# Kernel optimization log

Measured on AMD Instinct MI355X. Metric: run time of the kernel, lower is better.

The kernel has to match this reference:

```python
import jax, jax.numpy as jnp
from jax import lax
import numpy as np

SIGMA = 25.0
NUM_STEPS = 100
DT = 0.01
SQRT_DT = float(np.sqrt(DT))


def _score(x, eig, t, cond, W1, we, wt, b1, Wc, W2, b2):
    # x: [B,S,H], eig: [B,S], t: scalar, cond: [B,S,H] or None
    h = x @ W1 + eig[..., None] * we + t * wt + b1
    if cond is not None:
        h = h + cond @ Wc
    h = jax.nn.silu(h)
    return h @ W2 + b2


def _diffuse(x_T, eigvals, eigvecs, cond, params, key):
    # reverse SDE from t=1 to t=0 in NUM_STEPS steps
    ts = jnp.linspace(1.0, 0.0, NUM_STEPS)
    keys = jax.random.split(key, NUM_STEPS)
    VT = jnp.swapaxes(eigvecs, -2, -1)  # [B,S,S]

    def step(x, tk):
        t, k = tk
        x_spec = VT @ x                                   # spectral projection [B,S,H]
        score = _score(x_spec, eigvals, t, cond, *params)
        drift = -(SIGMA ** (2.0 * t)) * score
        noise = jax.random.normal(k, x.shape, x.dtype)
        x_new = x - drift * DT + (SIGMA ** t) * SQRT_DT * noise
        return x_new, None

    x, _ = lax.scan(step, x_T, (ts, keys))
    return x


def _make_net(key, H, scale):
    k = jax.random.split(key, 4)
    return dict(
        W1=jax.random.normal(k[0], (H, H), jnp.float32) * scale,
        we=jax.random.normal(k[1], (H,), jnp.float32) * scale,
        wt=jax.random.normal(k[2], (H,), jnp.float32) * scale,
        b1=jnp.zeros((H,), jnp.float32),
        Wc=jax.random.normal(k[3], (H, H), jnp.float32) * scale,
        W2=jax.random.normal(jax.random.fold_in(key, 99), (H, H), jnp.float32) * scale,
        b2=jnp.zeros((H,), jnp.float32),
    )


def setup_inputs() -> dict:
    key = jax.random.key(0)
    B, S, H = 4, 512, 256
    ks = jax.random.split(key, 9)
    inp = {}
    inp['features_text'] = jax.random.normal(ks[0], (B, S, H), jnp.float32)
    inp['features_audio'] = jax.random.normal(ks[1], (B, S, H), jnp.float32)
    inp['features_visual'] = jax.random.normal(ks[2], (B, S, H), jnp.float32)
    sg = jax.random.normal(ks[3], (B, S, S), jnp.float32)
    inp['speaker_graph'] = 0.5 * (sg + jnp.swapaxes(sg, -2, -1))  # symmetric for eigh
    tg = jax.random.normal(ks[4], (B, S, S), jnp.float32)
    inp['temporal_graph'] = 0.5 * (tg + jnp.swapaxes(tg, -2, -1))
    # only text modality (index 0) is missing -> diffusion path for text only
    inp['missing_mask'] = jnp.zeros((B, S, 3), bool).at[:, :, 0].set(True)
    inp['x_T'] = jax.random.normal(ks[5], (B, S, H), jnp.float32)
    scale = 1.0 / np.sqrt(H)
    for prefix, k in [('ts', ks[6]), ('tt', ks[7])]:  # text_speaker / text_temporal nets
        net = _make_net(k, H, scale)
        for name, v in net.items():
            inp[f'{prefix}_{name}'] = v
    kr = jax.random.split(ks[8], 2)
    inp['rec_W'] = jax.random.normal(kr[0], (H, H), jnp.float32) * scale
    inp['rec_b'] = jnp.zeros((H,), jnp.float32)
    return inp


def reference(features_text, features_audio, features_visual,
              speaker_graph, temporal_graph, missing_mask, x_T,
              ts_W1, ts_we, ts_wt, ts_b1, ts_Wc, ts_W2, ts_b2,
              tt_W1, tt_we, tt_wt, tt_b1, tt_Wc, tt_W2, tt_b2,
              rec_W, rec_b):
    # spectral decomposition of both graphs
    s_vals, s_vecs = jnp.linalg.eigh(speaker_graph)
    t_vals, t_vecs = jnp.linalg.eigh(temporal_graph)

    feats = {'text': features_text, 'audio': features_audio, 'visual': features_visual}
    miss = np.asarray(missing_mask)  # concrete branching as in torch forward
    any_missing = [bool(miss[:, :, i].any()) for i in range(3)]

    params = {'text': (
        (ts_W1, ts_we, ts_wt, ts_b1, ts_Wc, ts_W2, ts_b2),
        (tt_W1, tt_we, tt_wt, tt_b1, tt_Wc, tt_W2, tt_b2))}
    key = jax.random.key(42)

    recovered = {}
    for i, modality in enumerate(['text', 'audio', 'visual']):
        if any_missing[i]:
            # condition = mean of present (non-missing) other modalities
            cond_feats = [feats[m] for j, m in enumerate(['text', 'audio', 'visual'])
                          if m != modality and not any_missing[j]]
            cond = None
            if cond_feats:
                cond = jnp.mean(jnp.stack(cond_feats, axis=-1), axis=-1)
            k_s, k_t = jax.random.split(jax.random.fold_in(key, i))
            p_s, p_t = params[modality]
            x_s = _diffuse(x_T, s_vals, s_vecs, cond, p_s, k_s)
            x_t = _diffuse(x_T, t_vals, t_vecs, cond, p_t, k_t)
            rec = 0.5 * (x_s + x_t)
            recovered[modality] = rec @ rec_W + rec_b
        else:
            recovered[modality] = feats[modality]
    return (recovered['text'], recovered['audio'], recovered['visual'])
```

## Files before the change

kernel.cpp:

```cpp
#include <hip/hip_runtime.h>
#include <math.h>
#include <stdint.h>


#define NT 256
#define SZF 131072
#define MATSZ 262144
#define NB 16
#define ILAST 384
#define TBASE (ILAST+1)
#define TSZ (512-TBASE)

#define BD_DK   0
#define BD_ZK   4096
#define BD_RZK  8192
#define BD_TAU  12288
#define BD_DS   16384
#define BD_RHO  20480
#define BD_KSK  20736
#define BD_KIDX 22784
#define BD_DIDX 24832
#define BD_PERM 26880
#define BD_CNT  28928

#define ALD(p)    __hip_atomic_load((p),  __ATOMIC_RELAXED, __HIP_MEMORY_SCOPE_AGENT)
#define AST(p,v)  __hip_atomic_store((p), (v), __ATOMIC_RELAXED, __HIP_MEMORY_SCOPE_AGENT)

__host__ __device__ static inline unsigned rotl32(unsigned v, int r){ return (v<<r)|(v>>(32-r)); }

__host__ __device__ static inline void tf2x32(unsigned k0, unsigned k1,
                                              unsigned x0, unsigned x1,
                                              unsigned* o0, unsigned* o1){
  unsigned ks2 = k0 ^ k1 ^ 0x1BD11BDAu;
  x0 += k0; x1 += k1;
#define TF4(r0,r1,r2,r3) \
  x0 += x1; x1 = rotl32(x1,r0); x1 ^= x0; \
  x0 += x1; x1 = rotl32(x1,r1); x1 ^= x0; \
  x0 += x1; x1 = rotl32(x1,r2); x1 ^= x0; \
  x0 += x1; x1 = rotl32(x1,r3); x1 ^= x0;
  TF4(13,15,26,6)  x0 += k1;  x1 += ks2 + 1u;
  TF4(17,29,16,24) x0 += ks2; x1 += k0 + 2u;
  TF4(13,15,26,6)  x0 += k0;  x1 += k1 + 3u;
  TF4(17,29,16,24) x0 += k1;  x1 += ks2 + 4u;
  TF4(13,15,26,6)  x0 += ks2; x1 += k0 + 5u;
#undef TF4
  *o0 = x0; *o1 = x1;
}

__device__ static inline float erfinv_xla(float x){
  float w = -log1pf(-x*x);
  float p;
  if (w < 5.0f){
    w -= 2.5f;
    p = 2.81022636e-08f;
    p = fmaf(p, w, 3.43273939e-07f);
    p = fmaf(p, w, -3.5233877e-06f);
    p = fmaf(p, w, -4.39150654e-06f);
    p = fmaf(p, w, 0.00021858087f);
    p = fmaf(p, w, -0.00125372503f);
    p = fmaf(p, w, -0.00417768164f);
    p = fmaf(p, w, 0.246640727f);
    p = fmaf(p, w, 1.50140941f);
  } else {
    w = sqrtf(w) - 3.0f;
    p = -0.000200214257f;
    p = fmaf(p, w, 0.000100950558f);
    p = fmaf(p, w, 0.00134934322f);
    p = fmaf(p, w, -0.00367342844f);
    p = fmaf(p, w, 0.00573950773f);
    p = fmaf(p, w, -0.0076224613f);
    p = fmaf(p, w, 0.00943887047f);
    p = fmaf(p, w, 1.00167406f);
    p = fmaf(p, w, 2.83297682f);
  }
  return p*x;
}

__device__ static inline float bits_to_normal(unsigned bits){
  const float MINV = -0.99999994f;
  float f = __uint_as_float((bits >> 9) | 0x3f800000u) - 1.0f;
  float u = fmaxf(MINV, fmaf(f, 2.0f, MINV));
  return 1.41421356237309515f * erfinv_xla(u);
}

__device__ __forceinline__ void gbar2(unsigned* slots, int sg, int g, unsigned epoch,
                                      int* sdead){
  __threadfence_block();
  __syncthreads();
  int t = threadIdx.x;
  if (t == 0) AST(slots + (sg*NB + g)*16, epoch);
  if (t < NB && !*sdead){
    unsigned* sl = slots + (sg*NB + t)*16;
    int spins = 0;
    while (ALD(sl) < epoch){
      if (++spins > (1<<24)){ *sdead = 1; break; }
      if ((spins & 3) == 0) __builtin_amdgcn_s_sleep(1);
    }
  }
  __syncthreads();
}

__global__ __launch_bounds__(256) void k_sytd2_lds(const float* Gs, const float* Gt,
                                                   double* Vb, double* smalls,
                                                   unsigned* slots, double* Atail){
  int sg = blockIdx.x / NB, g = blockIdx.x % NB;
  const float* G = (sg < 4) ? (Gs + (size_t)sg*MATSZ) : (Gt + (size_t)(sg-4)*MATSZ);
  double* V = Vb + (size_t)sg*MATSZ;
  double* d  = smalls + (size_t)sg*512;
  double* e  = smalls + 4096 + (size_t)sg*512;
  double* tu = smalls + 8192 + (size_t)sg*512;
  double* acc0 = smalls + 274688 + (size_t)sg*512;
  double* acc1 = acc0 + 4096;
  double* col0 = smalls + 282880 + (size_t)sg*512;
  double* col1 = col0 + 4096;
  double* vvh  = smalls + 291072 + (size_t)sg*512;
  double* At = Atail + (size_t)sg*MATSZ;
  int t = threadIdx.x, wave = t >> 6, lane = t & 63;

  __shared__ double Arows[32][512];
  __shared__ double vv[512], wv[512], col2[512], acc[512];
  __shared__ double red[4];
  __shared__ double bc[4];
  __shared__ int sdead;

  if (t == 0) sdead = 0;

  for (int j=0; j<32; j++){
    int r = NB*j + g;
    for (int c=t; c<512; c+=256)
      Arows[j][c] = (double)G[(size_t)r*512 + c];
  }

  for (int r=t; r<512; r+=256) col2[r] = (r>=1) ? (double)G[(size_t)r*512] : 0.0;
  __syncthreads();
  {
    double part = 0.0;
    for (int r=2+t; r<512; r+=256) part += col2[r]*col2[r];
    #pragma unroll
    for (int off=32; off; off>>=1) part += __shfl_down(part, off, 64);
    if (lane==0) red[wave]=part;
    __syncthreads();
    if (t==0){
      double xsq = red[0]+red[1]+red[2]+red[3];
      double alpha = col2[1];
      double beta,tv,scal;
      if (xsq == 0.0){ beta=alpha; tv=0.0; scal=0.0; }
      else {
        beta = -copysign(sqrt(alpha*alpha + xsq), alpha);
        tv = (beta - alpha)/beta;
        scal = 1.0/(alpha - beta);
      }
      if (g==0){ e[0]=beta; tu[0]=tv; }
      bc[0]=tv; bc[1]=scal;
    }
  }
  __syncthreads();
  double tauv = bc[0];
  {
    double scal = bc[1];
    for (int r=t; r<512; r+=256){
      double v = 0.0;
      if (r==1) v = 1.0;
      else if (r>1) v = (tauv==0.0) ? 0.0 : col2[r]*scal;
      vv[r]=v;
      if (r>=1 && (r & (NB-1))==g) V[r] = v;
    }
  }
  __syncthreads();
  if (g==0){
    for (int r=1+t; r<512; r+=256) AST(&col0[r], (double)G[(size_t)r*512 + 1]);
  }
  {
    int r0 = 1 + ((g - 1) & (NB-1));
    for (int r = r0 + NB*wave; r < 512; r += 4*NB){
      const double* Ar = Arows[r>>4];
      double p = 0.0;
      for (int c=lane; c<512; c+=64) p += Ar[c]*vv[c];
      #pragma unroll
      for (int off=32; off; off>>=1) p += __shfl_down(p, off, 64);
      if (lane==0) AST(&acc0[r], p);
    }
  }

  for (int i=0; i<ILAST; i++){
    gbar2(slots, sg, g, (unsigned)(i+1), &sdead);
    int lo=i+1, lo2=i+2;
    double* accR = (i&1) ? acc1 : acc0;
    double* colR = (i&1) ? col1 : col0;
    double* accW = (i&1) ? acc0 : acc1;
    double* colW = (i&1) ? col0 : col1;
    double part = 0.0;
    for (int r=lo+t; r<512; r+=256){
      double a_ = ALD(&accR[r]);
      double c_ = ALD(&colR[r]);
      acc[r]=a_; col2[r]=c_;
      part += (tauv*a_)*vv[r];
    }
    #pragma unroll
    for (int off=32; off; off>>=1) part += __shfl_down(part, off, 64);
    if (lane==0) red[wave]=part;
    __syncthreads();
    {
      double dot = red[0]+red[1]+red[2]+red[3];
      double alpha2 = -0.5*tauv*dot;
      double vlo = vv[lo];
      double wlo = fma(alpha2, vlo, tauv*acc[lo]);
      for (int r=lo+t; r<512; r+=256){
        double wr = fma(alpha2, vv[r], tauv*acc[r]);
        wv[r]=wr;
        col2[r] = col2[r] - vv[r]*wlo - wr*vlo;
      }
    }
    __syncthreads();
    part = 0.0;
    for (int r=lo2+1+t; r<512; r+=256) part += col2[r]*col2[r];
    #pragma unroll
    for (int off=32; off; off>>=1) part += __shfl_down(part, off, 64);
    if (lane==0) red[wave]=part;
    __syncthreads();
    double tau2, scal2;
    {
      double xsq = red[0]+red[1]+red[2]+red[3];
      double alpha = col2[lo2];
      double beta;
      if (xsq == 0.0){ beta=alpha; tau2=0.0; scal2=0.0; }
      else {
        beta = -copysign(sqrt(alpha*alpha + xsq), alpha);
        tau2 = (beta - alpha)/beta;
        scal2 = 1.0/(alpha - beta);
      }
      if (t==0 && g==0){ e[lo]=beta; tu[lo]=tau2; }
    }
    {
      double vvc[8], wvc[8], v2c[8];
      #pragma unroll
      for (int j=0;j<8;j++){
        int c = lo + lane + 64*j;
        bool ok = c < 512;
        vvc[j] = ok ? vv[c] : 0.0;
        wvc[j] = ok ? wv[c] : 0.0;
        double v2v = 0.0;
        if (ok){
          if (c==lo2) v2v = 1.0;
          else if (c>lo2) v2v = (tau2==0.0) ? 0.0 : col2[c]*scal2;
        }
        v2c[j] = v2v;
      }
      int r0 = lo + ((g - lo) & (NB-1));
      for (int r = r0 + NB*wave; r < 512; r += 4*NB){
        double* Ar = Arows[r>>4];
        double vr = vv[r], wr = wv[r];
        double p = 0.0;
        #pragma unroll
        for (int j=0;j<8;j++){
          int c = lo + lane + 64*j;
          if (c < 512){
            double an = Ar[c] - vr*wvc[j] - wr*vvc[j];
            Ar[c] = an;
            p += an * v2c[j];
            if (c == lo2) AST(&colW[r], an);
          }
        }
        #pragma unroll
        for (int off=32; off; off>>=1) p += __shfl_down(p, off, 64);
        if (lane==0) AST(&accW[r], p);
      }
    }
    __syncthreads();
    for (int r=t; r<512; r+=256){
      double v = 0.0;
      if (r==lo2) v = 1.0;
      else if (r>lo2) v = (tau2==0.0) ? 0.0 : col2[r]*scal2;
      vv[r]=v;
      if (r>=lo2 && (r & (NB-1))==g) V[(size_t)lo*512 + r] = v;
    }
    tauv = tau2;
  }

  if (t < 32){
    int r = NB*t + g;
    if (r <= ILAST) d[r] = Arows[t][r];
  }
  for (int j=0; j<32; j++){
    int r = NB*j + g;
    if (r >= TBASE){
      for (int c=TBASE+t; c<512; c+=256)
        At[(size_t)r*512 + c] = Arows[j][c];
    }
  }
  if (g==0){
    for (int r=t; r<512; r+=256) vvh[r] = vv[r];
  }
}

__global__ __launch_bounds__(256) void k_sy_tail(const double* Atail, double* Vb,
                                                 double* smalls){
  int sg = blockIdx.x;
  double* V = Vb + (size_t)sg*MATSZ;
  double* d  = smalls + (size_t)sg*512;
  double* e  = smalls + 4096 + (size_t)sg*512;
  double* tu = smalls + 8192 + (size_t)sg*512;
  const double* accG = smalls + 274688 + (size_t)sg*512;
  const double* colG = smalls + 282880 + (size_t)sg*512;
  const double* vvG  = smalls + 291072 + (size_t)sg*512;
  const double* At0 = Atail + (size_t)sg*MATSZ;
  int t = threadIdx.x, wave = t >> 6, lane = t & 63;

  __shared__ double At[TSZ*128];
  __shared__ double vv[512], wv[512], col2[512], acc[512], accN[512], colN[512];
  __shared__ double red[4];

  for (int rl=0; rl<TSZ; rl++)
    for (int cl=t; cl<TSZ; cl+=256)
      At[rl*128+cl] = At0[(size_t)(TBASE+rl)*512 + TBASE+cl];
  for (int r=t; r<512; r+=256){
    if (r >= ILAST){ vv[r]=vvG[r]; acc[r]=accG[r]; col2[r]=colG[r]; }
  }
  double tauv = tu[ILAST];
  __syncthreads();

  for (int i=ILAST; i<510; i++){
    int lo=i+1, lo2=i+2;
    double part = 0.0;
    for (int r=lo+t; r<512; r+=256) part += (tauv*acc[r])*vv[r];
    #pragma unroll
    for (int off=32; off; off>>=1) part += __shfl_down(part, off, 64);
    if (lane==0) red[wave]=part;
    __syncthreads();
    {
      double dot = red[0]+red[1]+red[2]+red[3];
      double alpha2 = -0.5*tauv*dot;
      double vlo = vv[lo];
      double wlo = fma(alpha2, vlo, tauv*acc[lo]);
      for (int r=lo+t; r<512; r+=256){
        double wr = fma(alpha2, vv[r], tauv*acc[r]);
        wv[r]=wr;
        col2[r] = col2[r] - vv[r]*wlo - wr*vlo;
      }
    }
    __syncthreads();
    part = 0.0;
    for (int r=lo2+1+t; r<512; r+=256) part += col2[r]*col2[r];
    #pragma unroll
    for (int off=32; off; off>>=1) part += __shfl_down(part, off, 64);
    if (lane==0) red[wave]=part;
    __syncthreads();
    double tau2, scal2;
    {
      double xsq = red[0]+red[1]+red[2]+red[3];
      double alpha = col2[lo2];
      double beta;
      if (xsq == 0.0){ beta=alpha; tau2=0.0; scal2=0.0; }
      else {
        beta = -copysign(sqrt(alpha*alpha + xsq), alpha);
        tau2 = (beta - alpha)/beta;
        scal2 = 1.0/(alpha - beta);
      }
      if (t==0){ e[lo]=beta; tu[lo]=tau2; }
    }
    {
      double vvc[8], wvc[8], v2c[8];
      #pragma unroll
      for (int j=0;j<8;j++){
        int c = lo + lane + 64*j;
        bool ok = c < 512;
        vvc[j] = ok ? vv[c] : 0.0;
        wvc[j] = ok ? wv[c] : 0.0;
        double v2v = 0.0;
        if (ok){
          if (c==lo2) v2v = 1.0;
          else if (c>lo2) v2v = (tau2==0.0) ? 0.0 : col2[c]*scal2;
        }
        v2c[j] = v2v;
      }
      for (int r = lo + wave; r < 512; r += 4){
        double* Ar = &At[(r-TBASE)*128];
        double vr = vv[r], wr = wv[r];
        double p = 0.0;
        #pragma unroll
        for (int j=0;j<8;j++){
          int c = lo + lane + 64*j;
          if (c < 512){
            double an = Ar[c-TBASE] - vr*wvc[j] - wr*vvc[j];
            Ar[c-TBASE] = an;
            p += an * v2c[j];
            if (c == lo2) colN[r] = an;
          }
        }
        #pragma unroll
        for (int off=32; off; off>>=1) p += __shfl_down(p, off, 64);
        if (lane==0) accN[r] = p;
      }
    }
    __syncthreads();
    for (int r=t; r<512; r+=256){
      if (r >= lo2){
        double v = (r==lo2) ? 1.0 : ((tau2==0.0) ? 0.0 : col2[r]*scal2);
        vv[r]=v;
        V[(size_t)lo*512 + r] = v;
        col2[r] = colN[r];
        acc[r] = accN[r];
      }
    }
    tauv = tau2;
    __syncthreads();
  }
  for (int rl=t; rl<TSZ; rl+=256) d[TBASE+rl] = At[rl*128+rl];
}

__global__ void k_scale(double* smalls, int sbase){
  int sg = sbase + blockIdx.x, t = threadIdx.x;
  double* d = smalls + (size_t)sg*512;
  double* e = smalls + 4096 + (size_t)sg*512;
  __shared__ double red[256];
  double m = 0.0;
  for (int i=t;i<512;i+=256) m = fmax(m, fabs(d[i]));
  for (int i=t;i<511;i+=256) m = fmax(m, fabs(e[i]));
  red[t]=m; __syncthreads();
  for (int off=128; off; off>>=1){ if (t<off) red[t]=fmax(red[t],red[t+off]); __syncthreads(); }
  double org = red[0]; if (org == 0.0) org = 1.0;
  if (t==0) smalls[12288+sg] = org;
  double inv = 1.0/org;
  __syncthreads();
  for (int i=t;i<512;i+=256) d[i] *= inv;
  for (int i=t;i<511;i+=256) e[i] *= inv;
  __syncthreads();
  if (t < 31){
    int k = t + 1;
    double ae = fabs(e[16*k - 1]);
    d[16*k - 1] -= ae;
    d[16*k]     -= ae;
  }
}

__global__ __launch_bounds__(256) void k_leaves(double* smalls, double* Zb, int sbase){
  __shared__ double LA[4][256];
  __shared__ double LQ[4][256];
  int t = threadIdx.x, w = t >> 6, lane = t & 63;
  int L = blockIdx.x*4 + w;
  int s_local = L >> 5;
  int sg = sbase + s_local;
  int leaf = L & 31;
  double* dd = smalls + (size_t)sg*512;
  double* ee = smalls + 4096 + (size_t)sg*512;
  double* Z = Zb + (size_t)s_local*MATSZ;
  int base = leaf*16;
  double* A = LA[w]; double* Q = LQ[w];

  for (int i=lane; i<256; i+=64){ A[i]=0.0; Q[i]=0.0; }
  __builtin_amdgcn_sched_barrier(0);
  if (lane < 16){ A[lane*17] = dd[base+lane]; Q[lane*17] = 1.0; }
  if (lane < 15){
    double ev = ee[base+lane];
    A[lane*16+lane+1] = ev; A[(lane+1)*16+lane] = ev;
  }
  __builtin_amdgcn_sched_barrier(0);
  double nr = 0.0;
  if (lane == 0){ for (int i=0;i<256;i++) nr += A[i]*A[i]; }
  nr = __shfl(nr, 0, 64);
  double thr = nr*1e-30 + 1e-300;

  for (int sweep=0; sweep<60; sweep++){
    double offs = 0.0;
    for (int p=0;p<15;p++) for (int q=p+1;q<16;q++){
      double apq = A[p*16+q];
      offs += 2.0*apq*apq;
      if (apq == 0.0) continue;
      double theta = 0.5*(A[q*17]-A[p*17])/apq;
      double tt;
      if (fabs(theta) > 1e18) tt = 0.5/theta;
      else tt = copysign(1.0, theta)/(fabs(theta)+sqrt(theta*theta+1.0));
      double cc = 1.0/sqrt(tt*tt+1.0), ss = tt*cc;
      __builtin_amdgcn_sched_barrier(0);
      if (lane < 16){
        int k = lane;
        double akp=A[k*16+p], akq=A[k*16+q];
        A[k*16+p] = cc*akp - ss*akq;
        A[k*16+q] = ss*akp + cc*akq;
      }
      __builtin_amdgcn_sched_barrier(0);
      if (lane < 16){
        int k = lane;
        double apk=A[p*16+k], aqk=A[q*16+k];
        A[p*16+k] = cc*apk - ss*aqk;
        A[q*16+k] = ss*apk + cc*aqk;
      }
      __builtin_amdgcn_sched_barrier(0);
      if (lane < 16){
        int k = lane;
        double qkp=Q[k*16+p], qkq=Q[k*16+q];
        Q[k*16+p] = cc*qkp - ss*qkq;
        Q[k*16+q] = ss*qkp + cc*qkq;
      }
      __builtin_amdgcn_sched_barrier(0);
    }
    if (offs < thr) break;
  }
  __builtin_amdgcn_sched_barrier(0);
  if (lane == 0){
    for (int i=0;i<16;i++){
      int mi=i;
      for (int j=i+1;j<16;j++) if (A[j*17] < A[mi*17]) mi=j;
      if (mi!=i){
        double tmp=A[i*17]; A[i*17]=A[mi*17]; A[mi*17]=tmp;
        for (int k=0;k<16;k++){ double q1=Q[k*16+i]; Q[k*16+i]=Q[k*16+mi]; Q[k*16+mi]=q1; }
      }
    }
  }
  __builtin_amdgcn_sched_barrier(0);
  if (lane < 16) dd[base+lane] = A[lane*17];
  for (int i=lane; i<256; i+=64){
    int r = i >> 4, c = i & 15;
    Z[(size_t)(base+r)*512 + base + c] = Q[i];
  }
}

__global__ __launch_bounds__(256) void k_deflate(double* smalls, const double* Zsrc_b,
                                                 double* bscr, int level, int sbase){
  const double EPS32 = 5.9604644775390625e-8;
  const double ISQ2  = 0.70710678118654752440;
  int s_local = blockIdx.x;
  int sg = sbase + s_local;
  int hh = 16 << level, n = hh << 1;
  int merge = blockIdx.y, start = merge*n;
  double* d = smalls + (size_t)sg*512;
  const double* e = smalls + 4096 + (size_t)sg*512;
  const double* Z = Zsrc_b + (size_t)s_local*MATSZ;
  double* rotg = smalls + 12544 + (size_t)(sg*32+merge)*1024;
  double* dkG  = bscr + BD_DK  + (size_t)s_local*512 + start;
  double* zkG  = bscr + BD_ZK  + (size_t)s_local*512 + start;
  double* rzkG = bscr + BD_RZK + (size_t)s_local*512 + start;
  double* dsG  = bscr + BD_DS  + (size_t)s_local*512 + start;
  double* rhoG = bscr + BD_RHO;
  int* kidxG = (int*)(bscr + BD_KIDX) + s_local*512 + start;
  int* didxG = (int*)(bscr + BD_DIDX) + s_local*512 + start;
  int* permG = (int*)(bscr + BD_PERM) + s_local*512 + start;
  int* cntG  = (int*)(bscr + BD_CNT) + (s_local*32+merge)*2;

  __shared__ double ds[512], zl[512];
  __shared__ double rc[256], rs[256];
  __shared__ double red[256];
  __shared__ double sv[2];
  __shared__ int perm[512], kidx[512], didx[512];
  __shared__ int rp[256], rq[256];
  __shared__ int counts[2];
  int t = threadIdx.x;
  if (t == 0){
    int i=0, j=hh, k=0;
    while (i < hh && j < n){
      if (d[start+i] <= d[start+j]) perm[k++]=i++; else perm[k++]=j++;
    }
    while (i < hh) perm[k++]=i++;
    while (j < n)  perm[k++]=j++;
  }
  __syncthreads();
  double eb = e[start+hh-1];
  double rho = 2.0*fabs(eb);
  double sgn = (eb < 0.0) ? -1.0 : 1.0;
  for (int i=t; i<n; i+=NT){
    int p = perm[i];
    ds[i] = d[start+p];
    double zr = (p < hh) ? Z[(size_t)(start+hh-1)*512 + start + p]
                         : sgn * Z[(size_t)(start+hh)*512 + start + p];
    zl[i] = zr * ISQ2;
  }
  __syncthreads();
  double m = 0.0;
  for (int i=t;i<n;i+=NT) m = fmax(m, fabs(zl[i]));
  red[t]=m; __syncthreads();
  for (int off=128; off; off>>=1){ if (t<off) red[t]=fmax(red[t],red[t+off]); __syncthreads(); }
  if (t==0) sv[0] = red[0];
  __syncthreads();
  m = 0.0;
  for (int i=t;i<n;i+=NT) m = fmax(m, fabs(ds[i]));
  red[t]=m; __syncthreads();
  for (int off=128; off; off>>=1){ if (t<off) red[t]=fmax(red[t],red[t+off]); __syncthreads(); }
  if (t==0) sv[1] = red[0];
  __syncthreads();
  double zmaxv = sv[0];
  double tol = 8.0*EPS32*fmax(sv[1], zmaxv);

  if (t == 0){
    int K=0, nd=0, nrot=0;
    if (rho*zmaxv <= tol){
      for (int j=0;j<n;j++) didx[nd++]=j;
    } else {
      int pj = -1;
      for (int j=0;j<n;j++){
        if (rho*fabs(zl[j]) <= tol){
          didx[nd++]=j;
        } else if (pj < 0){
          pj = j;
        } else {
          double s_ = zl[pj], c_ = zl[j];
          double tau2 = sqrt(c_*c_ + s_*s_);
          double tdf = ds[j] - ds[pj];
          double cc = c_/tau2, sr = -s_/tau2;
          if (fabs(tdf*cc*sr) <= tol){
            zl[j] = tau2; zl[pj] = 0.0;
            if (nrot < 256){
              rp[nrot]=perm[pj]; rq[nrot]=perm[j]; rc[nrot]=cc; rs[nrot]=sr; nrot++;
            }
            double tn = ds[pj]*cc*cc + ds[j]*sr*sr;
            ds[j]  = ds[pj]*sr*sr + ds[j]*cc*cc;
            ds[pj] = tn;
            didx[nd++] = pj;
            pj = j;
          } else {
            kidx[K++] = pj;
            pj = j;
          }
        }
      }
      if (pj >= 0) kidx[K++] = pj;
    }
    for (int a=1;a<nd;a++){
      int v = didx[a]; double dv = ds[v]; int b = a-1;
      while (b >= 0 && ds[didx[b]] > dv){ didx[b+1]=didx[b]; b--; }
      didx[b+1] = v;
    }
    counts[0]=K; counts[1]=nd;
    cntG[0]=K; cntG[1]=nd;
    rhoG[s_local*32+merge] = rho;
    rotg[0] = (double)nrot;
    for (int i=0;i<nrot;i++){
      rotg[1+4*i]=(double)rp[i]; rotg[2+4*i]=(double)rq[i];
      rotg[3+4*i]=rc[i]; rotg[4+4*i]=rs[i];
    }
  }
  __syncthreads();
  int K = counts[0], nd = counts[1];
  for (int k=t; k<K; k+=NT){
    int ki = kidx[k];
    double dv = ds[ki], zv = zl[ki];
    dkG[k]=dv; zkG[k]=zv; rzkG[k]=(rho*zv)*zv; kidxG[k]=ki;
  }
  for (int j=t; j<n;  j+=NT){ dsG[j]=ds[j]; permG[j]=perm[j]; }
  for (int j=t; j<nd; j+=NT) didxG[j]=didx[j];
}

__global__ __launch_bounds__(256) void k_bisect(double* bscr, int level, int split){
  int s_local = blockIdx.x;
  int hh = 16 << level, n = hh << 1;
  int merge = blockIdx.y, start = merge*n;
  const double* dkG  = bscr + BD_DK  + (size_t)s_local*512 + start;
  const double* zkG  = bscr + BD_ZK  + (size_t)s_local*512 + start;
  const double* rzkG = bscr + BD_RZK + (size_t)s_local*512 + start;
  double* taukG = bscr + BD_TAU + (size_t)s_local*512 + start;
  int* KskG = (int*)(bscr + BD_KSK) + s_local*512 + start;
  const int* cntG = (int*)(bscr + BD_CNT) + (s_local*32+merge)*2;
  double rho = (bscr + BD_RHO)[s_local*32+merge];
  __shared__ double dks[512], rzks[512], zks[512];
  int t = threadIdx.x;
  int K = cntG[0];
  for (int i=t;i<K;i+=NT){ dks[i]=dkG[i]; rzks[i]=rzkG[i]; zks[i]=zkG[i]; }
  __syncthreads();
  int lane = t & 63, w = t >> 6;
  for (int j2 = blockIdx.z*4 + w; j2 < K; j2 += split*4){
    int Kb; double lo, hi;
    if (j2 < K-1){
      double mid = 0.5*(dks[j2+1]-dks[j2]);
      double dj = dks[j2];
      double part = 0.0;
      for (int i=lane;i<K;i+=64){ double dif=(dks[i]-dj)-mid; part += rzks[i]/dif; }
      #pragma unroll
      for (int off=32; off; off>>=1) part += __shfl_xor(part, off, 64);
      double gg = 1.0 + part;
      if (gg >= 0.0){ Kb=j2;   lo=0.0;  hi=mid; }
      else          { Kb=j2+1; lo=-mid; hi=0.0; }
    } else {
      double part = 0.0;
      for (int i=lane;i<K;i+=64) part += zks[i]*zks[i];
      #pragma unroll
      for (int off=32; off; off>>=1) part += __shfl_xor(part, off, 64);
      Kb=K-1; lo=0.0; hi=rho*part + 1e-300;
    }
    double dK = dks[Kb];
    for (int it=0; it<72; it++){
      double mid = 0.5*(lo+hi);
      if (mid==lo || mid==hi) break;
      double part = 0.0;
      for (int i=lane;i<K;i+=64){ double dif=(dks[i]-dK)-mid; part += rzks[i]/dif; }
      #pragma unroll
      for (int off=32; off; off>>=1) part += __shfl_xor(part, off, 64);
      double gg = 1.0 + part;
      if (gg < 0.0) lo=mid; else hi=mid;
    }
    if (lane==0){ KskG[j2]=Kb; taukG[j2]=0.5*(lo+hi); }
  }
}

__global__ __launch_bounds__(256) void k_sfin(double* smalls, double* Sm_b,
                                              const double* bscr, int level, int sbase){
  int s_local = blockIdx.x;
  int sg = sbase + s_local;
  int hh = 16 << level, n = hh << 1;
  int merge = blockIdx.y, start = merge*n;
  double* d = smalls + (size_t)sg*512;
  double* Sm = Sm_b + (size_t)s_local*MATSZ;
  const double* rotg = smalls + 12544 + (size_t)(sg*32+merge)*1024;
  const double* dkG  = bscr + BD_DK  + (size_t)s_local*512 + start;
  const double* zkG  = bscr + BD_ZK  + (size_t)s_local*512 + start;
  const double* taukG= bscr + BD_TAU + (size_t)s_local*512 + start;
  const double* dsG  = bscr + BD_DS  + (size_t)s_local*512 + start;
  const int* KskG = (int*)(bscr + BD_KSK) + s_local*512 + start;
  const int* kidxG= (int*)(bscr + BD_KIDX) + s_local*512 + start;
  const int* didxG= (int*)(bscr + BD_DIDX) + s_local*512 + start;
  const int* permG= (int*)(bscr + BD_PERM) + s_local*512 + start;
  const int* cntG = (int*)(bscr + BD_CNT) + (s_local*32+merge)*2;
  double rho = (bscr + BD_RHO)[s_local*32+merge];
  __shared__ double dk[512], zk[512], tauk[512], zh[512], outlam[512], ds[512];
  __shared__ int Ksk[512], kidx[512], didx[512], perm[512], outid[512];
  int t = threadIdx.x;
  int K = cntG[0], nd = cntG[1];
  for (int i=t;i<K;i+=NT){
    dk[i]=dkG[i]; zk[i]=zkG[i]; tauk[i]=taukG[i]; Ksk[i]=KskG[i]; kidx[i]=kidxG[i];
  }
  for (int i=t;i<n;i+=NT){ ds[i]=dsG[i]; perm[i]=permG[i]; }
  for (int i=t;i<nd;i+=NT) didx[i]=didxG[i];
  __syncthreads();
  for (int i=t; i<K; i+=NT){
    double P = (Ksk[i]==i) ? tauk[i] : (dk[Ksk[i]]-dk[i]) + tauk[i];
    for (int j=0;j<K;j++){
      if (j==i) continue;
      double num = (dk[Ksk[j]]-dk[i]) + tauk[j];
      double den = dk[j]-dk[i];
      P *= num/den;
    }
    zh[i] = copysign(sqrt(fabs(P/rho)), zk[i]);
  }
  __syncthreads();
  if (t == 0){
    int a=0, b=0;
    for (int j=0;j<n;j++){
      double la = (a<K)  ? (dk[Ksk[a]]+tauk[a]) : 1e300;
      double lb = (b<nd) ? ds[didx[b]]          : 1e300;
      if (la <= lb){ outid[j]=a;     outlam[j]=la; a++; }
      else         { outid[j]=512+b; outlam[j]=lb; b++; }
    }
  }
  __syncthreads();
  for (int j=t; j<n; j+=NT) d[start+j] = outlam[j];
  for (int j=t; j<n; j+=NT){
    double* col = Sm + (size_t)(start+j)*512;
    int id = outid[j];
    for (int i=0;i<n;i++) col[i]=0.0;
    if (id >= 512){
      col[perm[didx[id-512]]] = 1.0;
    } else {
      int k = id;
      double ss_ = 0.0;
      for (int i=0;i<K;i++){
        double dif = (dk[i]-dk[Ksk[k]]) - tauk[k];
        if (dif == 0.0) dif = 1e-300;
        double v = zh[i]/dif;
        col[perm[kidx[i]]] = v; ss_ += v*v;
      }
      double inv = 1.0/sqrt(ss_);
      for (int i=0;i<K;i++) col[perm[kidx[i]]] *= inv;
    }
  }
  int cnt = (int)rotg[0];
  if (cnt > 0){
    for (int j=t; j<n; j+=NT){
      double* col = Sm + (size_t)(start+j)*512;
      for (int i=cnt-1; i>=0; i--){
        int p = (int)rotg[1+4*i], q = (int)rotg[2+4*i];
        double c = rotg[3+4*i], sr = rotg[4+4*i];
        double a = col[p], b = col[q];
        col[p] = c*a - sr*b;
        col[q] = sr*a + c*b;
      }
    }
  }
}

__global__ __launch_bounds__(256) void k_gemm64(const double* Zsrc_b, const double* Sm_b,
                                                double* Zdst_b, int level){
  int hh = 16 << level, n = hh << 1;
  int mpm = 512 / n;
  int bz = blockIdx.z;
  int s = bz / mpm, merge = bz % mpm;
  int start = merge*n;
  const double* Zs = Zsrc_b + (size_t)s*MATSZ;
  const double* Sm = Sm_b + (size_t)s*MATSZ;
  double* Zd = Zdst_b + (size_t)s*MATSZ;
  int row0 = start + blockIdx.y*32, col0 = start + blockIdx.x*32;
  int t = threadIdx.x;
  int tr = t >> 4, tc = t & 15;
  __shared__ double As[32][33];
  __shared__ double Bs[32][33];
  double a00=0,a01=0,a10=0,a11=0;
  for (int q0=0; q0<n; q0+=32){
    #pragma unroll
    for (int it=0; it<4; it++){
      int idx = t + it*256;
      int r = idx >> 5, q = idx & 31;
      As[r][q] = Zs[(size_t)(row0+r)*512 + start + q0 + q];
    }
    #pragma unroll
    for (int it=0; it<4; it++){
      int idx = t + it*256;
      int c = idx >> 5, q = idx & 31;
      Bs[q][c] = Sm[(size_t)(col0+c)*512 + q0 + q];
    }
    __syncthreads();
    #pragma unroll 8
    for (int q=0;q<32;q++){
      double ar0=As[tr][q], ar1=As[tr+16][q];
      double bc0=Bs[q][tc], bc1=Bs[q][tc+16];
      a00 = fma(ar0,bc0,a00); a01 = fma(ar0,bc1,a01);
      a10 = fma(ar1,bc0,a10); a11 = fma(ar1,bc1,a11);
    }
    __syncthreads();
  }
  Zd[(size_t)(row0+tr)*512 + col0+tc]       = a00;
  Zd[(size_t)(row0+tr)*512 + col0+tc+16]    = a01;
  Zd[(size_t)(row0+tr+16)*512 + col0+tc]    = a10;
  Zd[(size_t)(row0+tr+16)*512 + col0+tc+16] = a11;
}

__global__ __launch_bounds__(256) void k_backq(double* Z2_b, const double* Vh_b,
                                               const double* smalls, int sbase){
  int s_local = blockIdx.x, cb = blockIdx.y;
  int sg = sbase + s_local;
  double* Z = Z2_b + (size_t)s_local*MATSZ;
  const double* V = Vh_b + (size_t)sg*MATSZ;
  const double* tu = smalls + 8192 + (size_t)sg*512;
  int cg = threadIdx.x >> 5, lane = threadIdx.x & 31;
  int c = cb*8 + cg;
  __shared__ double zc[8][512];
  for (int r=lane; r<512; r+=32) zc[cg][r] = Z[(size_t)r*512 + c];
  for (int i=509; i>=0; i--){
    double tv = tu[i];
    if (tv == 0.0) continue;
    double wp = 0.0;
    for (int r=i+1+lane; r<512; r+=32) wp += V[(size_t)i*512 + r]*zc[cg][r];
    #pragma unroll
    for (int off=16; off; off>>=1) wp += __shfl_down(wp, off, 32);
    double w = __shfl(wp, 0, 32);
    double tw = tv*w;
    for (int r=i+1+lane; r<512; r+=32) zc[cg][r] -= tw*V[(size_t)i*512 + r];
  }
  for (int r=lane; r<512; r+=32) Z[(size_t)r*512 + c] = zc[cg][r];
}

__global__ void k_finalize(const double* Z2_b, const double* smalls,
                           float* Vs32, float* Vt32, float* eig, int sbase){
  int s_local = blockIdx.x;
  int sg = sbase + s_local;
  const double* Z = Z2_b + (size_t)s_local*MATSZ;
  float* Vt_pass = (sg < 4) ? (Vs32 + (size_t)sg*MATSZ)
                            : (Vt32 + (size_t)(sg-4)*MATSZ);
  double org = smalls[12288+sg];
  int idx = blockIdx.y*256 + threadIdx.x;
  int r = idx >> 9, c = idx & 511;
  Vt_pass[(size_t)c*512 + r] = (float)Z[(size_t)r*512 + c];
  if (idx < 512)
    eig[(size_t)sg*512 + idx] = (float)(smalls[(size_t)sg*512 + idx]*org);
}

struct KArgs {
  const float* Vt;
  const float* Vt2;
  float *xspec, *hbuf, *x, *E;
  const float *W1s, *W1t, *W2s, *W2t;
  const float *b2s, *b2t, *wts, *wtt, *b1s, *b1t, *wes, *wet;
  const float *cond, *Wcs, *Wct;
  const float *eig;
  const float *rec, *recW, *recb;
  float* out;
  float t, a, bc;
  unsigned nk0, nk1, nk2, nk3;
  int mode, nmat, ntx;
};

__global__ __launch_bounds__(256) void k_gemm32(KArgs P){
  int t = threadIdx.x;
  int L = blockIdx.x;
  int mat = L % P.nmat;
  int tile = L / P.nmat;
  int n0 = (tile % P.ntx) << 5;
  int m0 = (tile / P.ntx) << 6;
  const float *A, *B; float *C;
  int lda, K, chain = 0;
  if (P.mode == 0){
    A = (mat < 4) ? (P.Vt + (size_t)mat*MATSZ) : (P.Vt2 + (size_t)(mat-4)*MATSZ);
    lda = 512; K = 512;
    B = P.x + (size_t)mat*SZF; C = P.xspec + (size_t)mat*SZF;
  } else if (P.mode == 1){
    chain = mat >> 2;
    A = P.xspec + (size_t)mat*SZF; lda = 256; K = 256;
    B = chain ? P.W1t : P.W1s; C = P.hbuf + (size_t)mat*SZF;
  } else if (P.mode == 2){
    chain = mat >> 2;
    A = P.hbuf + (size_t)mat*SZF; lda = 256; K = 256;
    B = chain ? P.W2t : P.W2s; C = P.x + (size_t)mat*SZF;
  } else if (P.mode == 3){
    chain = mat;
    A = P.cond; lda = 256; K = 256;
    B = chain ? P.Wct : P.Wcs; C = P.E + (size_t)chain*4*SZF;
  } else {
    A = P.rec; lda = 256; K = 256;
    B = P.recW; C = P.out;
  }
  __shared__ float As[2][32][68];
  __shared__ float Bs[2][32][36];
  float acc[4][2] = {{0}};
  const int ra = t >> 2, kk4 = (t & 3) << 2;
  const int kb = (t & 127) >> 3, c4 = (t & 7) << 2;
  const int tr4 = (t >> 4) << 2, tc2 = (t & 15) << 1;
  const float* Aptr = &A[(size_t)(m0 + ra)*lda + kk4];
  const float* Bptr = &B[(size_t)kb*256 + n0 + c4];
  {
    const float4 av  = *(const float4*)Aptr;
    const float4 av2 = *(const float4*)(Aptr + 16);
    As[0][kk4+0][ra]=av.x;  As[0][kk4+1][ra]=av.y;  As[0][kk4+2][ra]=av.z;  As[0][kk4+3][ra]=av.w;
    As[0][16+kk4+0][ra]=av2.x; As[0][16+kk4+1][ra]=av2.y; As[0][16+kk4+2][ra]=av2.z; As[0][16+kk4+3][ra]=av2.w;
    if (t < 128){
      const float4 bv  = *(const float4*)Bptr;
      const float4 bv2 = *(const float4*)(Bptr + (size_t)16*256);
      *(float4*)&Bs[0][kb][c4] = bv;
      *(float4*)&Bs[0][kb+16][c4] = bv2;
    }
  }
  int buf = 0;
  for (int k0=0; k0<K; k0+=32){
    __syncthreads();
    bool more = (k0+32) < K;
    float4 avN, avN2, bvN, bvN2;
    if (more){
      avN  = *(const float4*)(Aptr + k0 + 32);
      avN2 = *(const float4*)(Aptr + k0 + 48);
      if (t < 128){
        bvN  = *(const float4*)(Bptr + (size_t)(k0+32)*256);
        bvN2 = *(const float4*)(Bptr + (size_t)(k0+48)*256);
      }
    }
    {
      const float (*Asb)[68] = As[buf];
      const float (*Bsb)[36] = Bs[buf];
      #pragma unroll
      for (int kk=0; kk<32; kk++){
        const float4 a4 = *(const float4*)&Asb[kk][tr4];
        const float2 b2 = *(const float2*)&Bsb[kk][tc2];
        const float ar[4] = {a4.x, a4.y, a4.z, a4.w};
        #pragma unroll
        for (int q=0;q<4;q++){
          acc[q][0] = fmaf(ar[q], b2.x, acc[q][0]);
          acc[q][1] = fmaf(ar[q], b2.y, acc[q][1]);
        }
      }
    }
    if (more){
      int nb = buf^1;
      As[nb][kk4+0][ra]=avN.x;  As[nb][kk4+1][ra]=avN.y;  As[nb][kk4+2][ra]=avN.z;  As[nb][kk4+3][ra]=avN.w;
      As[nb][16+kk4+0][ra]=avN2.x; As[nb][16+kk4+1][ra]=avN2.y; As[nb][16+kk4+2][ra]=avN2.z; As[nb][16+kk4+3][ra]=avN2.w;
      if (t < 128){
        *(float4*)&Bs[nb][kb][c4] = bvN;
        *(float4*)&Bs[nb][kb+16][c4] = bvN2;
      }
      buf = nb;
    }
  }
  #pragma unroll
  for (int q=0;q<4;q++){
    int r = m0 + tr4 + q;
    size_t rowoff = (size_t)r*256 + n0 + tc2;
    float2 cv;
    if (P.mode == 2) cv = *(const float2*)&C[rowoff];
    float res[2];
    #pragma unroll
    for (int p=0;p<2;p++){
      int c = n0 + tc2 + p;
      size_t oi = (size_t)r*256 + c;
      float v = acc[q][p];
      if (P.mode == 1){
        v += P.E[(size_t)mat*SZF + oi] + P.t * ((chain ? P.wtt : P.wts)[c]);
        float sg = 1.0f/(1.0f + expf(-v));
        v = v * sg;
      } else if (P.mode == 2){
        float bias = (chain ? P.b2t : P.b2s)[c];
        unsigned j = ((unsigned)(mat & 3))*131072u + (unsigned)oi;
        unsigned kk0 = chain ? P.nk2 : P.nk0;
        unsigned kk1 = chain ? P.nk3 : P.nk1;
        unsigned y0, y1;
        tf2x32(kk0, kk1, 0u, j, &y0, &y1);
        float nz = bits_to_normal(y0 ^ y1);
        float cx = (p==0) ? cv.x : cv.y;
        v = cx + P.a*(v + bias) + P.bc*nz;
      } else if (P.mode == 3){
        int bb = r >> 9, s2 = r & 511;
        v += (chain ? P.b1t : P.b1s)[c]
           + P.eig[(size_t)(chain*4 + bb)*512 + s2] * ((chain ? P.wet : P.wes)[c]);
      } else if (P.mode == 4){
        v += P.recb[c];
      }
      res[p] = v;
    }
    *(float2*)&C[rowoff] = make_float2(res[0], res[1]);
  }
}

__global__ void k_init(float* cond, float* x, const float* a, const float* v,
                       const float* xT){
  size_t i = (size_t)blockIdx.x*256 + threadIdx.x;
  size_t b = i >> 17, off = i & 131071;
  x[i] = xT[((b & 3) << 17) + off];
  if (i < 524288) cond[i] = 0.5f*(a[i] + v[i]);
}

__global__ void k_recc(float* rec, const float* x, float* out,
                       const float* a, const float* v){
  size_t i = (size_t)blockIdx.x*256 + threadIdx.x;
  if (i < 524288) rec[i] = 0.5f*(x[i] + x[i + 524288]);
  out[524288 + i] = (i < 524288) ? a[i] : v[i - 524288];
}

extern "C" void kernel_launch(void* const* d_in, const int* in_sizes, int n_in,
                              void* d_out, int out_size, void* d_ws, size_t ws_size,
                              hipStream_t stream){
  const float* f_audio   = (const float*)d_in[1];
  const float* f_visual  = (const float*)d_in[2];
  const float* g_speaker = (const float*)d_in[3];
  const float* g_temporal= (const float*)d_in[4];
  const float* x_T       = (const float*)d_in[6];
  const float* tsW1=(const float*)d_in[7],  *tswe=(const float*)d_in[8],
             * tswt=(const float*)d_in[9],  *tsb1=(const float*)d_in[10],
             * tsWc=(const float*)d_in[11], *tsW2=(const float*)d_in[12],
             * tsb2=(const float*)d_in[13];
  const float* ttW1=(const float*)d_in[14], *ttwe=(const float*)d_in[15],
             * ttwt=(const float*)d_in[16], *ttb1=(const float*)d_in[17],
             * ttWc=(const float*)d_in[18], *ttW2=(const float*)d_in[19],
             * ttb2=(const float*)d_in[20];
  const float* recW=(const float*)d_in[21], *recb=(const float*)d_in[22];
  float* out = (float*)d_out;

  const size_t MB = 1ull << 20;
  if (ws_size < 43*MB) return;
  bool wide = ws_size >= 80*MB;

  char* ws = (char*)d_ws;
  double* Vh     = (double*)(ws + 0);
  double* Atail  = (double*)(ws + 16*MB);
  double* A64    = (double*)(ws + 16*MB);
  double* Zb     = wide ? (double*)(ws + 48*MB) : (double*)(ws + 24*MB);
  double* Sm     = wide ? (double*)(ws + 64*MB) : (double*)(ws + 32*MB);
  double* smalls = (double*)(ws + 40*MB);
  unsigned* slots = (unsigned*)(smalls + 295168);
  float* Vt32_s  = (float*)(ws + 0);
  float* Vt32_t  = (float*)(ws + 8*MB);
  float* eig32   = (float*)(ws + 42*MB + 512*1024);
  double* bscr   = (double*)(ws + 42*MB + 640*1024);
  float* cond  = (float*)(ws + 16*MB);
  float* E     = (float*)(ws + 18*MB);
  float* xall  = (float*)(ws + 22*MB);
  float* xspec = (float*)(ws + 26*MB);
  float* hbuf  = (float*)(ws + 30*MB);

  unsigned f0, f1;
  tf2x32(0u, 42u, 0u, 0u, &f0, &f1);
  unsigned s0,s1,t0,t1;
  tf2x32(f0, f1, 0u, 0u, &s0, &s1);
  tf2x32(f0, f1, 0u, 1u, &t0, &t1);
  unsigned skeys[100][2], tkeys[100][2];
  for (int k=0; k<100; k++){
    tf2x32(s0, s1, 0u, (unsigned)k, &skeys[k][0], &skeys[k][1]);
    tf2x32(t0, t1, 0u, (unsigned)k, &tkeys[k][0], &tkeys[k][1]);
  }

  hipMemsetAsync(slots, 0, 16384, stream);

  k_sytd2_lds<<<8*NB, 256, 0, stream>>>(g_speaker, g_temporal, Vh, smalls, slots, Atail);
  k_sy_tail<<<8, 256, 0, stream>>>(Atail, Vh, smalls);

  int npass = wide ? 1 : 2;
  int nmat  = wide ? 8 : 4;
  for (int pass=0; pass<npass; pass++){
    int sbase = wide ? 0 : 4*pass;
    k_scale<<<nmat, 256, 0, stream>>>(smalls, sbase);
    hipMemsetAsync(Zb, 0, (size_t)(wide?16:8)*MB, stream);
    hipMemsetAsync(A64, 0, (size_t)(wide?16:8)*MB, stream);
    k_leaves<<<nmat*8, 256, 0, stream>>>(smalls, Zb, sbase);
    for (int level=0; level<5; level++){
      int n = 32 << level, mpm = 512/n;
      double* src = (level & 1) ? A64 : Zb;
      double* dst = (level & 1) ? Zb  : A64;
      int split = 2 << level;
      k_deflate<<<dim3(nmat, mpm), 256, 0, stream>>>(smalls, src, bscr, level, sbase);
      k_bisect<<<dim3(nmat, mpm, split), 256, 0, stream>>>(bscr, level, split);
      k_sfin<<<dim3(nmat, mpm), 256, 0, stream>>>(smalls, Sm, bscr, level, sbase);
      k_gemm64<<<dim3(n/32, n/32, nmat*mpm), 256, 0, stream>>>(src, Sm, dst, level);
    }
    k_backq<<<dim3(nmat, 64), 256, 0, stream>>>(A64, Vh, smalls, sbase);
    k_finalize<<<dim3(nmat, 1024), 256, 0, stream>>>(A64, smalls,
                                                     Vt32_s, Vt32_t, eig32, sbase);
  }

  k_init<<<4096, 256, 0, stream>>>(cond, xall, f_audio, f_visual, x_T);

  KArgs P;
  P.Vt = Vt32_s; P.Vt2 = Vt32_t;
  P.xspec = xspec; P.hbuf = hbuf; P.x = xall; P.E = E;
  P.W1s = tsW1; P.W1t = ttW1; P.W2s = tsW2; P.W2t = ttW2;
  P.b2s = tsb2; P.b2t = ttb2; P.wts = tswt; P.wtt = ttwt;
  P.b1s = tsb1; P.b1t = ttb1; P.wes = tswe; P.wet = ttwe;
  P.cond = cond; P.Wcs = tsWc; P.Wct = ttWc;
  P.eig = eig32; P.rec = xspec; P.recW = recW; P.recb = recb; P.out = out;
  P.t = 0.f; P.a = 0.f; P.bc = 0.f;
  P.nk0 = 0; P.nk1 = 0; P.nk2 = 0; P.nk3 = 0;
  P.ntx = 8;

  P.mode = 3; P.nmat = 2;
  k_gemm32<<<512, 256, 0, stream>>>(P);

  for (int k=0; k<100; k++){
    float tf = (float)(1.0 - (double)k/99.0);
    float av = (float)(pow(25.0, 2.0*(double)tf) * 0.01);
    float bcv = (float)(pow(25.0, (double)tf) * 0.1);
    P.nk0 = skeys[k][0]; P.nk1 = skeys[k][1];
    P.nk2 = tkeys[k][0]; P.nk3 = tkeys[k][1];
    P.nmat = 8;
    P.mode = 0;
    k_gemm32<<<512, 256, 0, stream>>>(P);
    P.mode = 1; P.t = tf;
    k_gemm32<<<512, 256, 0, stream>>>(P);
    P.mode = 2; P.a = av; P.bc = bcv;
    k_gemm32<<<512, 256, 0, stream>>>(P);
  }

  k_recc<<<4096, 256, 0, stream>>>(xspec, xall, out, f_audio, f_visual);
  P.mode = 4; P.nmat = 1;
  k_gemm32<<<256, 256, 0, stream>>>(P);
}
```

Before: 14.17 ms.

## Fuse score MLP GEMMs into one kernel and tile the eigvec transpose

Replaces the two per-step GEMM launches (x_spec@W1 with SiLU, then h@W2 with noise update) with one fused kernel. Each block keeps an 8-row strip of x_spec and the hidden activations in LDS, so the hidden buffer never goes to global memory. It also rewrites the finalize transpose to use a 32x32 LDS tile for coalesced writes, and merges the Givens rotation loop into the eigenvector-construction loop. The tradeoff is lower parallelism per block: 8 rows per block, with W1/W2 re-streamed by every block.

Result: slower. 18.03 ms (+27.2%).

```diff
diff --git a/kernel.cpp b/kernel.cpp
--- a/kernel.cpp
+++ b/kernel.cpp
@@ -741,6 +741,7 @@
   }
   __syncthreads();
   for (int j=t; j<n; j+=NT) d[start+j] = outlam[j];
+  int cnt = (int)rotg[0];
   for (int j=t; j<n; j+=NT){
     double* col = Sm + (size_t)(start+j)*512;
     int id = outid[j];
@@ -759,18 +760,12 @@
       double inv = 1.0/sqrt(ss_);
       for (int i=0;i<K;i++) col[perm[kidx[i]]] *= inv;
     }
-  }
-  int cnt = (int)rotg[0];
-  if (cnt > 0){
-    for (int j=t; j<n; j+=NT){
-      double* col = Sm + (size_t)(start+j)*512;
-      for (int i=cnt-1; i>=0; i--){
-        int p = (int)rotg[1+4*i], q = (int)rotg[2+4*i];
-        double c = rotg[3+4*i], sr = rotg[4+4*i];
-        double a = col[p], b = col[q];
-        col[p] = c*a - sr*b;
-        col[q] = sr*a + c*b;
-      }
+    for (int i=cnt-1; i>=0; i--){
+      int p = (int)rotg[1+4*i], q = (int)rotg[2+4*i];
+      double c = rotg[3+4*i], sr = rotg[4+4*i];
+      double a = col[p], b = col[q];
+      col[p] = c*a - sr*b;
+      col[q] = sr*a + c*b;
     }
   }
 }
@@ -852,26 +847,42 @@
   const double* Z = Z2_b + (size_t)s_local*MATSZ;
   float* Vt_pass = (sg < 4) ? (Vs32 + (size_t)sg*MATSZ)
                             : (Vt32 + (size_t)(sg-4)*MATSZ);
-  double org = smalls[12288+sg];
-  int idx = blockIdx.y*256 + threadIdx.x;
-  int r = idx >> 9, c = idx & 511;
-  Vt_pass[(size_t)c*512 + r] = (float)Z[(size_t)r*512 + c];
-  if (idx < 512)
-    eig[(size_t)sg*512 + idx] = (float)(smalls[(size_t)sg*512 + idx]*org);
+  int t = threadIdx.x;
+  int tr = blockIdx.y & 15, tc = blockIdx.y >> 4;
+  __shared__ float ft[32][33];
+  {
+    int i = t >> 3, j4 = (t & 7) << 2;
+    const double* zr = &Z[(size_t)(tr*32 + i)*512 + tc*32 + j4];
+    ft[i][j4+0] = (float)zr[0];
+    ft[i][j4+1] = (float)zr[1];
+    ft[i][j4+2] = (float)zr[2];
+    ft[i][j4+3] = (float)zr[3];
+  }
+  __syncthreads();
+  {
+    int j = t >> 3, i4 = (t & 7) << 2;
+    float* vr = &Vt_pass[(size_t)(tc*32 + j)*512 + tr*32 + i4];
+    vr[0] = ft[i4+0][j];
+    vr[1] = ft[i4+1][j];
+    vr[2] = ft[i4+2][j];
+    vr[3] = ft[i4+3][j];
+  }
+  if (blockIdx.y == 0){
+    double org = smalls[12288+sg];
+    for (int idx=t; idx<512; idx+=256)
+      eig[(size_t)sg*512 + idx] = (float)(smalls[(size_t)sg*512 + idx]*org);
+  }
 }
 
 struct KArgs {
   const float* Vt;
   const float* Vt2;
-  float *xspec, *hbuf, *x, *E;
-  const float *W1s, *W1t, *W2s, *W2t;
-  const float *b2s, *b2t, *wts, *wtt, *b1s, *b1t, *wes, *wet;
+  float *xspec, *x, *E;
+  const float *b1s, *b1t, *wes, *wet;
   const float *cond, *Wcs, *Wct;
   const float *eig;
   const float *rec, *recW, *recb;
   float* out;
-  float t, a, bc;
-  unsigned nk0, nk1, nk2, nk3;
   int mode, nmat, ntx;
 };
 
@@ -888,14 +899,6 @@
     A = (mat < 4) ? (P.Vt + (size_t)mat*MATSZ) : (P.Vt2 + (size_t)(mat-4)*MATSZ);
     lda = 512; K = 512;
     B = P.x + (size_t)mat*SZF; C = P.xspec + (size_t)mat*SZF;
-  } else if (P.mode == 1){
-    chain = mat >> 2;
-    A = P.xspec + (size_t)mat*SZF; lda = 256; K = 256;
-    B = chain ? P.W1t : P.W1s; C = P.hbuf + (size_t)mat*SZF;
-  } else if (P.mode == 2){
-    chain = mat >> 2;
-    A = P.hbuf + (size_t)mat*SZF; lda = 256; K = 256;
-    B = chain ? P.W2t : P.W2s; C = P.x + (size_t)mat*SZF;
   } else if (P.mode == 3){
     chain = mat;
     A = P.cond; lda = 256; K = 256;
@@ -967,29 +970,12 @@
   for (int q=0;q<4;q++){
     int r = m0 + tr4 + q;
     size_t rowoff = (size_t)r*256 + n0 + tc2;
-    float2 cv;
-    if (P.mode == 2) cv = *(const float2*)&C[rowoff];
     float res[2];
     #pragma unroll
     for (int p=0;p<2;p++){
       int c = n0 + tc2 + p;
-      size_t oi = (size_t)r*256 + c;
       float v = acc[q][p];
-      if (P.mode == 1){
-        v += P.E[(size_t)mat*SZF + oi] + P.t * ((chain ? P.wtt : P.wts)[c]);
-        float sg = 1.0f/(1.0f + expf(-v));
-        v = v * sg;
-      } else if (P.mode == 2){
-        float bias = (chain ? P.b2t : P.b2s)[c];
-        unsigned j = ((unsigned)(mat & 3))*131072u + (unsigned)oi;
-        unsigned kk0 = chain ? P.nk2 : P.nk0;
-        unsigned kk1 = chain ? P.nk3 : P.nk1;
-        unsigned y0, y1;
-        tf2x32(kk0, kk1, 0u, j, &y0, &y1);
-        float nz = bits_to_normal(y0 ^ y1);
-        float cx = (p==0) ? cv.x : cv.y;
-        v = cx + P.a*(v + bias) + P.bc*nz;
-      } else if (P.mode == 3){
+      if (P.mode == 3){
         int bb = r >> 9, s2 = r & 511;
         v += (chain ? P.b1t : P.b1s)[c]
            + P.eig[(size_t)(chain*4 + bb)*512 + s2] * ((chain ? P.wet : P.wes)[c]);
@@ -999,6 +985,148 @@
       res[p] = v;
     }
     *(float2*)&C[rowoff] = make_float2(res[0], res[1]);
+  }
+}
+
+struct KFuse {
+  const float *xspec, *E;
+  float* x;
+  const float *W1s, *W1t, *W2s, *W2t;
+  const float *b2s, *b2t, *wts, *wtt;
+  float t, a, bc;
+  unsigned nk0, nk1, nk2, nk3;
+};
+
+__global__ __launch_bounds__(256) void k_fuse12(KFuse S){
+  int t = threadIdx.x;
+  int mat = blockIdx.x & 7;
+  int row0 = (blockIdx.x >> 3) << 3;
+  int chain = mat >> 2;
+  const float* xsp_g = S.xspec + (size_t)mat*SZF;
+  float* xg = S.x + (size_t)mat*SZF;
+  const float* W1 = chain ? S.W1t : S.W1s;
+  const float* W2 = chain ? S.W2t : S.W2s;
+  const float* Eb = S.E + (size_t)mat*SZF;
+  const float* wt = chain ? S.wtt : S.wts;
+  const float* b2 = chain ? S.b2t : S.b2s;
+
+  __shared__ float xs[8][264];
+  __shared__ float hl[8][264];
+  __shared__ float Bt[2][16][264];
+
+  const int kb = t >> 4, cb = (t & 15) << 4;
+  const int rr = t >> 5, c4 = (t & 31) << 2;
+
+  {
+    float4 v0 = *(const float4*)&xsp_g[(size_t)(row0 + rr)*256 + c4];
+    float4 v1 = *(const float4*)&xsp_g[(size_t)(row0 + rr)*256 + c4 + 128];
+    *(float4*)&xs[rr][c4] = v0;
+    *(float4*)&xs[rr][c4+128] = v1;
+  }
+  #pragma unroll
+  for (int j=0;j<4;j++)
+    *(float4*)&Bt[0][kb][cb + 4*j] = *(const float4*)&W1[(size_t)kb*256 + cb + 4*j];
+
+  float acc[8];
+  #pragma unroll
+  for (int j=0;j<8;j++) acc[j]=0.f;
+  int cur = 0;
+  for (int k0=0; k0<256; k0+=16){
+    __syncthreads();
+    bool more = (k0+16) < 256;
+    float4 pw[4];
+    if (more){
+      #pragma unroll
+      for (int j=0;j<4;j++)
+        pw[j] = *(const float4*)&W1[(size_t)(k0+16+kb)*256 + cb + 4*j];
+    }
+    #pragma unroll
+    for (int kk=0; kk<16; kk++){
+      float a = xs[rr][k0+kk];
+      const float4 b0 = *(const float4*)&Bt[cur][kk][c4];
+      const float4 b1 = *(const float4*)&Bt[cur][kk][c4+128];
+      acc[0]=fmaf(a,b0.x,acc[0]); acc[1]=fmaf(a,b0.y,acc[1]);
+      acc[2]=fmaf(a,b0.z,acc[2]); acc[3]=fmaf(a,b0.w,acc[3]);
+      acc[4]=fmaf(a,b1.x,acc[4]); acc[5]=fmaf(a,b1.y,acc[5]);
+      acc[6]=fmaf(a,b1.z,acc[6]); acc[7]=fmaf(a,b1.w,acc[7]);
+    }
+    if (more){
+      int nb = cur^1;
+      #pragma unroll
+      for (int j=0;j<4;j++) *(float4*)&Bt[nb][kb][cb+4*j] = pw[j];
+      cur = nb;
+    }
+  }
+  {
+    int rg = row0 + rr;
+    const float4 e0 = *(const float4*)&Eb[(size_t)rg*256 + c4];
+    const float4 e1 = *(const float4*)&Eb[(size_t)rg*256 + c4 + 128];
+    const float ev[8] = {e0.x,e0.y,e0.z,e0.w,e1.x,e1.y,e1.z,e1.w};
+    #pragma unroll
+    for (int j=0;j<8;j++){
+      int c = (j<4) ? (c4 + j) : (c4 + 128 + j - 4);
+      float v = acc[j];
+      v += ev[j] + S.t * wt[c];
+      float sg = 1.0f/(1.0f + expf(-v));
+      hl[rr][c] = v * sg;
+    }
+  }
+  __syncthreads();
+  #pragma unroll
+  for (int j=0;j<4;j++)
+    *(float4*)&Bt[0][kb][cb + 4*j] = *(const float4*)&W2[(size_t)kb*256 + cb + 4*j];
+  #pragma unroll
+  for (int j=0;j<8;j++) acc[j]=0.f;
+  cur = 0;
+  for (int k0=0; k0<256; k0+=16){
+    __syncthreads();
+    bool more = (k0+16) < 256;
+    float4 pw[4];
+    if (more){
+      #pragma unroll
+      for (int j=0;j<4;j++)
+        pw[j] = *(const float4*)&W2[(size_t)(k0+16+kb)*256 + cb + 4*j];
+    }
+    #pragma unroll
+    for (int kk=0; kk<16; kk++){
+      float a = hl[rr][k0+kk];
+      const float4 b0 = *(const float4*)&Bt[cur][kk][c4];
+      const float4 b1 = *(const float4*)&Bt[cur][kk][c4+128];
+      acc[0]=fmaf(a,b0.x,acc[0]); acc[1]=fmaf(a,b0.y,acc[1]);
+      acc[2]=fmaf(a,b0.z,acc[2]); acc[3]=fmaf(a,b0.w,acc[3]);
+      acc[4]=fmaf(a,b1.x,acc[4]); acc[5]=fmaf(a,b1.y,acc[5]);
+      acc[6]=fmaf(a,b1.z,acc[6]); acc[7]=fmaf(a,b1.w,acc[7]);
+    }
+    if (more){
+      int nb = cur^1;
+      #pragma unroll
+      for (int j=0;j<4;j++) *(float4*)&Bt[nb][kb][cb+4*j] = pw[j];
+      cur = nb;
+    }
+  }
+  {
+    unsigned kk0 = chain ? S.nk2 : S.nk0;
+    unsigned kk1 = chain ? S.nk3 : S.nk1;
+    int rg = row0 + rr;
+    const float4 x0 = *(const float4*)&xg[(size_t)rg*256 + c4];
+    const float4 x1 = *(const float4*)&xg[(size_t)rg*256 + c4 + 128];
+    const float cx[8] = {x0.x,x0.y,x0.z,x0.w,x1.x,x1.y,x1.z,x1.w};
+    float res[8];
+    #pragma unroll
+    for (int j=0;j<8;j++){
+      int c = (j<4) ? (c4 + j) : (c4 + 128 + j - 4);
+      unsigned oi = (unsigned)rg*256u + (unsigned)c;
+      float v = acc[j];
+      float bias = b2[c];
+      unsigned jj = ((unsigned)(mat & 3))*131072u + oi;
+      unsigned y0, y1;
+      tf2x32(kk0, kk1, 0u, jj, &y0, &y1);
+      float nz = bits_to_normal(y0 ^ y1);
+      v = cx[j] + S.a*(v + bias) + S.bc*nz;
+      res[j] = v;
+    }
+    *(float4*)&xg[(size_t)rg*256 + c4]       = make_float4(res[0],res[1],res[2],res[3]);
+    *(float4*)&xg[(size_t)rg*256 + c4 + 128] = make_float4(res[4],res[5],res[6],res[7]);
   }
 }
 
@@ -1056,7 +1184,6 @@
   float* E     = (float*)(ws + 18*MB);
   float* xall  = (float*)(ws + 22*MB);
   float* xspec = (float*)(ws + 26*MB);
-  float* hbuf  = (float*)(ws + 30*MB);
 
   unsigned f0, f1;
   tf2x32(0u, 42u, 0u, 0u, &f0, &f1);
@@ -1093,40 +1220,38 @@
       k_gemm64<<<dim3(n/32, n/32, nmat*mpm), 256, 0, stream>>>(src, Sm, dst, level);
     }
     k_backq<<<dim3(nmat, 64), 256, 0, stream>>>(A64, Vh, smalls, sbase);
-    k_finalize<<<dim3(nmat, 1024), 256, 0, stream>>>(A64, smalls,
-                                                     Vt32_s, Vt32_t, eig32, sbase);
+    k_finalize<<<dim3(nmat, 256), 256, 0, stream>>>(A64, smalls,
+                                                    Vt32_s, Vt32_t, eig32, sbase);
   }
 
   k_init<<<4096, 256, 0, stream>>>(cond, xall, f_audio, f_visual, x_T);
 
   KArgs P;
   P.Vt = Vt32_s; P.Vt2 = Vt32_t;
-  P.xspec = xspec; P.hbuf = hbuf; P.x = xall; P.E = E;
-  P.W1s = tsW1; P.W1t = ttW1; P.W2s = tsW2; P.W2t = ttW2;
-  P.b2s = tsb2; P.b2t = ttb2; P.wts = tswt; P.wtt = ttwt;
+  P.xspec = xspec; P.x = xall; P.E = E;
   P.b1s = tsb1; P.b1t = ttb1; P.wes = tswe; P.wet = ttwe;
   P.cond = cond; P.Wcs = tsWc; P.Wct = ttWc;
   P.eig = eig32; P.rec = xspec; P.recW = recW; P.recb = recb; P.out = out;
-  P.t = 0.f; P.a = 0.f; P.bc = 0.f;
-  P.nk0 = 0; P.nk1 = 0; P.nk2 = 0; P.nk3 = 0;
   P.ntx = 8;
 
   P.mode = 3; P.nmat = 2;
   k_gemm32<<<512, 256, 0, stream>>>(P);
 
+  KFuse S;
+  S.xspec = xspec; S.E = E; S.x = xall;
+  S.W1s = tsW1; S.W1t = ttW1; S.W2s = tsW2; S.W2t = ttW2;
+  S.b2s = tsb2; S.b2t = ttb2; S.wts = tswt; S.wtt = ttwt;
+
+  P.mode = 0; P.nmat = 8;
   for (int k=0; k<100; k++){
     float tf = (float)(1.0 - (double)k/99.0);
     float av = (float)(pow(25.0, 2.0*(double)tf) * 0.01);
     float bcv = (float)(pow(25.0, (double)tf) * 0.1);
-    P.nk0 = skeys[k][0]; P.nk1 = skeys[k][1];
-    P.nk2 = tkeys[k][0]; P.nk3 = tkeys[k][1];
-    P.nmat = 8;
-    P.mode = 0;
     k_gemm32<<<512, 256, 0, stream>>>(P);
-    P.mode = 1; P.t = tf;
-    k_gemm32<<<512, 256, 0, stream>>>(P);
-    P.mode = 2; P.a = av; P.bc = bcv;
-    k_gemm32<<<512, 256, 0, stream>>>(P);
+    S.t = tf; S.a = av; S.bc = bcv;
+    S.nk0 = skeys[k][0]; S.nk1 = skeys[k][1];
+    S.nk2 = tkeys[k][0]; S.nk3 = tkeys[k][1];
+    k_fuse12<<<512, 256, 0, stream>>>(S);
   }
 
   k_recc<<<4096, 256, 0, stream>>>(xspec, xall, out, f_audio, f_visual);
```
